# Kernel optimization log

Hardware: AMD Instinct MI355X
Metric: run time of the kernel (lower is better)

The kernel has to match this reference:

```python
import math
import jax, jax.numpy as jnp
import numpy as np

H = 16  # head_count

def setup_inputs() -> dict:
    key = jax.random.key(0)
    ks = jax.random.split(key, 7)
    B, S, D = 2, 2048, 1024
    query = jax.random.normal(ks[0], (B, S, D), dtype=jnp.float32)
    # mask: True = masked position (matches masked_fill_ semantics)
    mask = jax.random.randint(ks[1], (B, S, S), 0, 2) > 0
    scale = 1.0 / math.sqrt(D)  # xavier-ish init scale
    Wq = jax.random.normal(ks[2], (D, D), dtype=jnp.float32) * scale
    Wk = jax.random.normal(ks[3], (D, D), dtype=jnp.float32) * scale
    Wv = jax.random.normal(ks[4], (D, D), dtype=jnp.float32) * scale
    Wo = jax.random.normal(ks[5], (D, D), dtype=jnp.float32) * scale
    bo = jnp.zeros((D,), dtype=jnp.float32)
    return {"query": query, "mask": mask, "Wq": Wq, "Wk": Wk, "Wv": Wv, "Wo": Wo, "bo": bo}


def reference(query, mask, Wq, Wk, Wv, Wo, bo):
    B, S, D = query.shape
    dh = D // H

    def split_heads(x):  # [B,S,D] -> [B,H,S,dh]
        return x.reshape(B, S, H, dh).transpose(0, 2, 1, 3)

    # torch nn.Linear computes x @ W.T (bias-free for q/k/v)
    q = split_heads(query @ Wq.T) * (1.0 / math.sqrt(dh))
    k = split_heads(query @ Wk.T)
    v = split_heads(query @ Wv.T)

    scores = jnp.einsum('bhqd,bhkd->bhqk', q, k)           # [B,H,S,S]
    scores = jnp.where(mask[:, None, :, :], jnp.float32(-1e18), scores)
    weights = jax.nn.softmax(scores, axis=-1)               # dropout=0 -> identity
    ctx = jnp.einsum('bhqk,bhkd->bhqd', weights, v)         # [B,H,S,dh]
    ctx = ctx.transpose(0, 2, 1, 3).reshape(B, S, D)        # combine heads
    return ctx @ Wo.T + bo
```

## Files before the change

### kernel.cpp

```cpp
#include <hip/hip_runtime.h>

#define S_LEN 2048
#define D_MODEL 1024
#define NH 16
#define DH 64

typedef __bf16 bf16x8 __attribute__((ext_vector_type(8)));
typedef __bf16 bf16x4 __attribute__((ext_vector_type(4)));
typedef float f32x4 __attribute__((ext_vector_type(4)));
typedef unsigned short us8 __attribute__((ext_vector_type(8)));

__device__ __forceinline__ unsigned short f2bf(float f) {
  unsigned int x = __float_as_uint(f);
  x += 0x7fffu + ((x >> 16) & 1u);
  return (unsigned short)(x >> 16);
}

__device__ __forceinline__ bf16x4 cvt4(f32x4 v) {
  return __builtin_convertvector(v, bf16x4);
}

__device__ __forceinline__ float exp2raw(float x) {
#if __has_builtin(__builtin_amdgcn_exp2f)
  return __builtin_amdgcn_exp2f(x);
#else
  return exp2f(x);
#endif
}

__device__ __forceinline__ f32x4 mfma16(bf16x8 a, bf16x8 b, f32x4 c) {
  return __builtin_amdgcn_mfma_f32_16x16x32_bf16(a, b, c, 0, 0, 0);
}

__device__ __forceinline__ void gl2lds(const unsigned short* g, unsigned short* l) {
  __builtin_amdgcn_global_load_lds(
      (__attribute__((address_space(1))) void*)g,
      (__attribute__((address_space(3))) void*)l, 16, 0, 0);
}

__global__ __launch_bounds__(256) void prep_kernel(
    const float* __restrict__ q, const float* __restrict__ wq,
    const float* __restrict__ wk, const float* __restrict__ wv,
    const float* __restrict__ wo, const int* __restrict__ mask,
    unsigned short* __restrict__ qbf, unsigned short* __restrict__ wbf,
    unsigned long long* __restrict__ bits) {
  const int bx = blockIdx.x;
  if (bx < 32768) {
    int i = bx * 256 + threadIdx.x;
    unsigned long long bal = __ballot(mask[i] != 0);
    if ((threadIdx.x & 63) == 0) bits[i >> 6] = bal;
  } else {
    const long t = (long)(bx - 32768) * 256 + threadIdx.x;
    const float* src;
    unsigned short* dst;
    long e;
    if (t < 524288) { src = q; dst = qbf; e = t * 8; }
    else {
      long u = t - 524288;
      int wi = (int)(u >> 17);
      e = (u & 131071) * 8;
      src = wi == 0 ? wq : wi == 1 ? wk : wi == 2 ? wv : wo;
      dst = wbf + (long)wi * 1048576;
    }
    float4 a = *(const float4*)(src + e);
    float4 b = *(const float4*)(src + e + 4);
    ushort4 p0 = {f2bf(a.x), f2bf(a.y), f2bf(a.z), f2bf(a.w)};
    ushort4 p1 = {f2bf(b.x), f2bf(b.y), f2bf(b.z), f2bf(b.w)};
    *(ushort4*)(dst + e) = p0;
    *(ushort4*)(dst + e + 4) = p1;
  }
}

__global__ __launch_bounds__(256) void gemm_qkv(
    const unsigned short* __restrict__ A, const unsigned short* __restrict__ W3,
    unsigned short* __restrict__ qb, unsigned short* __restrict__ kb,
    unsigned short* __restrict__ vt, float qscale) {
  __shared__ __align__(16) char smemq[34816];
  unsigned short* As = (unsigned short*)smemq;
  unsigned short* Bs = (unsigned short*)(smemq + 16384);
  unsigned short* E = (unsigned short*)smemq;
  const int tid = threadIdx.x, lane = tid & 63, wid = tid >> 6;
  const int wm = wid >> 1, wn = wid & 1;
  const int quad = lane >> 4, c = lane & 15, cx = c & 7;
  const int nG = blockIdx.x * 128;
  const int wi = nG >> 10, nn0 = nG & 1023;
  const int m0 = blockIdx.y * 128;
  const unsigned short* Bsrc = W3 + (size_t)wi * 1048576;
  const int srow = lane >> 3;
  const int schk = ((lane & 7) ^ srow) * 8;
  const unsigned short* ag = A + (size_t)(m0 + wid * 32 + srow) * 1024 + schk;
  const unsigned short* bg = Bsrc + (size_t)(nn0 + wid * 32 + srow) * 1024 + schk;
  f32x4 acc[4][4] = {};
  for (int kk = 0; kk < 1024; kk += 64) {
#pragma unroll
    for (int i = 0; i < 4; ++i) {
      gl2lds(ag + (size_t)(i * 8) * 1024 + kk, &As[(wid * 32 + i * 8) * 64]);
      gl2lds(bg + (size_t)(i * 8) * 1024 + kk, &Bs[(wid * 32 + i * 8) * 64]);
    }
    __syncthreads();
#pragma unroll
    for (int kc = 0; kc < 2; ++kc) {
      bf16x8 a[4], b[4];
#pragma unroll
      for (int mt = 0; mt < 4; ++mt)
        a[mt] = *(const bf16x8*)(
            &As[(wm * 64 + mt * 16 + c) * 64 + ((kc * 4 + quad) ^ cx) * 8]);
#pragma unroll
      for (int nt = 0; nt < 4; ++nt)
        b[nt] = *(const bf16x8*)(
            &Bs[(wn * 64 + nt * 16 + c) * 64 + ((kc * 4 + quad) ^ cx) * 8]);
#pragma unroll
      for (int mt = 0; mt < 4; ++mt)
#pragma unroll
        for (int nt = 0; nt < 4; ++nt)
          acc[mt][nt] = mfma16(a[mt], b[nt], acc[mt][nt]);
    }
    __syncthreads();
  }

  const float scl = (wi == 0) ? qscale : 1.0f;
  if (wi < 2) {
#pragma unroll
    for (int mt = 0; mt < 4; ++mt)
#pragma unroll
      for (int nt = 0; nt < 4; ++nt) {
        const int sl = wm * 64 + mt * 16 + quad * 4;
        const int nl = wn * 64 + nt * 16 + c;
#pragma unroll
        for (int r = 0; r < 4; ++r)
          E[(sl + r) * 136 + nl] = f2bf(acc[mt][nt][r] * scl);
      }
  } else {
#pragma unroll
    for (int mt = 0; mt < 4; ++mt)
#pragma unroll
      for (int nt = 0; nt < 4; ++nt) {
        const int sl = wm * 64 + mt * 16 + quad * 4;
        const int nl = wn * 64 + nt * 16 + c;
        *(bf16x4*)(&E[nl * 136 + sl]) = cvt4(acc[mt][nt]);
      }
  }
  __syncthreads();
  {
    const int rl = tid >> 1, hf = tid & 1;
    const unsigned short* src = &E[rl * 136 + hf * 64];
    if (wi < 2) {
      const int mb = m0 + rl;
      const int bb = mb >> 11, ss = mb & 2047;
      const int hh = (nn0 + hf * 64) >> 6;
      unsigned short* dst = (wi == 0 ? qb : kb) +
                            (size_t)((bb * NH + hh) * S_LEN + ss) * DH;
#pragma unroll
      for (int j = 0; j < 8; ++j)
        *(us8*)(dst + j * 8) = *(const us8*)(src + j * 8);
    } else {
      const int n = nn0 + rl;
      const int hh = n >> 6, d = n & 63;
      const int bb = m0 >> 11, ss0 = (m0 & 2047) + hf * 64;
      unsigned short* dst =
          vt + (size_t)((bb * NH + hh) * DH + d) * S_LEN + ss0;
#pragma unroll
      for (int j = 0; j < 8; ++j)
        *(us8*)(dst + j * 8) = *(const us8*)(src + j * 8);
    }
  }
}

__global__ __launch_bounds__(256) void gemm_out(
    const unsigned short* __restrict__ A, const unsigned short* __restrict__ W,
    float* __restrict__ out, const float* __restrict__ bias) {
  __shared__ unsigned short As[128 * 128];
  __shared__ unsigned short Bs[64 * 128];
  const int tid = threadIdx.x, lane = tid & 63, wid = tid >> 6;
  const int wm = wid >> 1, wn = wid & 1;
  const int quad = lane >> 4, c = lane & 15, cx = c & 7;
  const int n0 = blockIdx.x * 64, m0 = blockIdx.y * 128;
  const int srow4 = lane >> 4, sch = lane & 15;
  const int co0 = (sch ^ srow4) * 8;
  const int co1 = (sch ^ (4 + srow4)) * 8;
  const unsigned short* agr = A + (size_t)(m0 + wid * 32 + srow4) * 1024;
  const unsigned short* bgr = W + (size_t)(n0 + wid * 16 + srow4) * 1024;
  f32x4 acc[4][2] = {};
  for (int kk = 0; kk < 1024; kk += 128) {
#pragma unroll
    for (int i = 0; i < 8; ++i)
      gl2lds(agr + (size_t)(i * 4) * 1024 + kk + ((i & 1) ? co1 : co0),
             &As[(wid * 32 + i * 4) * 128]);
#pragma unroll
    for (int i = 0; i < 4; ++i)
      gl2lds(bgr + (size_t)(i * 4) * 1024 + kk + ((i & 1) ? co1 : co0),
             &Bs[(wid * 16 + i * 4) * 128]);
    __syncthreads();
#pragma unroll
    for (int kc = 0; kc < 4; ++kc) {
      bf16x8 a[4], b[2];
#pragma unroll
      for (int mt = 0; mt < 4; ++mt)
        a[mt] = *(const bf16x8*)(
            &As[(wm * 64 + mt * 16 + c) * 128 + ((kc * 4 + quad) ^ cx) * 8]);
#pragma unroll
      for (int nt = 0; nt < 2; ++nt)
        b[nt] = *(const bf16x8*)(
            &Bs[(wn * 32 + nt * 16 + c) * 128 + ((kc * 4 + quad) ^ cx) * 8]);
#pragma unroll
      for (int mt = 0; mt < 4; ++mt)
#pragma unroll
        for (int nt = 0; nt < 2; ++nt)
          acc[mt][nt] = mfma16(a[mt], b[nt], acc[mt][nt]);
    }
    __syncthreads();
  }
#pragma unroll
  for (int mt = 0; mt < 4; ++mt) {
#pragma unroll
    for (int nt = 0; nt < 2; ++nt) {
      const int mb = m0 + wm * 64 + mt * 16 + quad * 4;
      const int n = n0 + wn * 32 + nt * 16 + c;
      const float bv = bias[n];
#pragma unroll
      for (int r = 0; r < 4; ++r)
        out[(size_t)(mb + r) * D_MODEL + n] = acc[mt][nt][r] + bv;
    }
  }
}

__global__ __launch_bounds__(256, 2) void attn_kernel(
    const unsigned short* __restrict__ qb, const unsigned short* __restrict__ kb,
    const unsigned short* __restrict__ vt,
    const unsigned long long* __restrict__ mbits,
    unsigned short* __restrict__ ctx) {
  const int h = blockIdx.x, qt = blockIdx.y, b = blockIdx.z;
  const int bh = b * NH + h;
  const int tid = threadIdx.x, lane = tid & 63, wid = tid >> 6;
  const int quad = lane >> 4, c = lane & 15, cx = c & 7;
  const int qw = wid & 1, kh = wid >> 1;
  const int q0 = qt * 128;
  __shared__ __align__(16) char smem[65536];
  unsigned short* KVb = (unsigned short*)smem;

  const int qbase = q0 + qw * 64;
  const unsigned short* qp = qb + (size_t)(bh * S_LEN + qbase + c) * DH;
  bf16x8 bq[4][2];
#pragma unroll
  for (int sub = 0; sub < 4; ++sub) {
    bq[sub][0] = *(const bf16x8*)(qp + sub * 16 * DH + quad * 8);
    bq[sub][1] = *(const bf16x8*)(qp + sub * 16 * DH + 32 + quad * 8);
  }

  const bf16x8 onesv = {(__bf16)1.f, (__bf16)1.f, (__bf16)1.f, (__bf16)1.f,
                        (__bf16)1.f, (__bf16)1.f, (__bf16)1.f, (__bf16)1.f};

  f32x4 o[4][4] = {};
  float lacc[4] = {0.f, 0.f, 0.f, 0.f};
  const unsigned long long* mq0 =
      mbits + (size_t)(b * S_LEN + qbase + c) * 32 + kh * 16;

  const int srow = lane >> 3, schk = ((lane & 7) ^ srow) * 8;

  const unsigned short* gKb =
      kb + (size_t)(bh * S_LEN + (wid & 1) * 1024) * DH + schk;
  const unsigned short* gV =
      vt + (size_t)(bh * DH + srow) * S_LEN + (wid - 2) * 1024 + schk;

  for (int kt = 0; kt < 1024; kt += 128) {
    if (wid < 2) {
#pragma unroll
      for (int hf = 0; hf < 2; ++hf)
#pragma unroll
        for (int i = 0; i < 8; ++i) {
          const int t = i * 8 + srow;
          const int st = (t & 0x23) | ((t >> 2) & 0x04) | ((t << 1) & 0x18);
          gl2lds(gKb + (size_t)(kt + hf * 64 + st) * DH,
                 &KVb[hf * 16384 + wid * 4096 + i * 512]);
        }
    } else {
#pragma unroll
      for (int hf = 0; hf < 2; ++hf)
#pragma unroll
        for (int i = 0; i < 8; ++i)
          gl2lds(gV + (size_t)(i * 8) * S_LEN + kt + hf * 64,
                 &KVb[hf * 16384 + wid * 4096 + i * 512]);
    }
    __syncthreads();

#pragma unroll
    for (int hf = 0; hf < 2; ++hf) {
      const unsigned short* Ksh = KVb + hf * 16384 + kh * 4096;
      const unsigned short* Vsh = KVb + hf * 16384 + (2 + kh) * 4096;
      const int mi = (kt >> 6) + hf;

      bf16x8 kf[8];
#pragma unroll
      for (int g = 0; g < 4; ++g) {
        const int rho = g * 16 + c;
        kf[2 * g] = *(const bf16x8*)(&Ksh[rho * 64 + (quad ^ cx) * 8]);
        kf[2 * g + 1] =
            *(const bf16x8*)(&Ksh[rho * 64 + ((4 + quad) ^ cx) * 8]);
      }

      bf16x8 bps[4][2];
#pragma unroll
      for (int sub = 0; sub < 4; ++sub) {
        f32x4 s[4];
        __builtin_amdgcn_s_setprio(1);
#pragma unroll
        for (int g = 0; g < 4; ++g) {
          f32x4 z = {};
          z = mfma16(kf[2 * g], bq[sub][0], z);
          z = mfma16(kf[2 * g + 1], bq[sub][1], z);
          s[g] = z;
        }
        __builtin_amdgcn_s_setprio(0);
        const unsigned long long w64 = mq0[sub * 512 + mi];
        const unsigned int wlo = (unsigned int)w64;
        const unsigned int whi = (unsigned int)(w64 >> 32);
        f32x4 p[4];
#pragma unroll
        for (int g = 0; g < 4; ++g) {
          const unsigned int bits =
              ((g & 2) ? whi : wlo) >> (quad * 8 + (g & 1) * 4);
#pragma unroll
          for (int r = 0; r < 4; ++r) {
            const float e = exp2raw(s[g][r]);
            p[g][r] = ((bits >> r) & 1u) ? 0.f : e;
          }
        }
        union { bf16x8 v; bf16x4 h[2]; } u0, u1;
        u0.h[0] = cvt4(p[0]); u0.h[1] = cvt4(p[1]);
        u1.h[0] = cvt4(p[2]); u1.h[1] = cvt4(p[3]);
        bps[sub][0] = u0.v;
        bps[sub][1] = u1.v;
        f32x4 zs = {};
        zs = mfma16(onesv, bps[sub][0], zs);
        zs = mfma16(onesv, bps[sub][1], zs);
        lacc[sub] += zs[0];
      }

      __builtin_amdgcn_s_setprio(1);
#pragma unroll
      for (int ks = 0; ks < 2; ++ks) {
#pragma unroll
        for (int nt = 0; nt < 4; ++nt) {
          bf16x8 av = *(const bf16x8*)(
              &Vsh[(nt * 16 + c) * 64 + ((ks * 4 + quad) ^ cx) * 8]);
#pragma unroll
          for (int sub = 0; sub < 4; ++sub)
            o[sub][nt] = mfma16(av, bps[sub][ks], o[sub][nt]);
        }
      }
      __builtin_amdgcn_s_setprio(0);
    }
    __syncthreads();
  }

  float* mrg = (float*)smem;
  float* ml = mrg + 8 * 1088;
  if (kh == 1) {
#pragma unroll
    for (int sub = 0; sub < 4; ++sub) {
      float* mo = mrg + (qw * 4 + sub) * 1088;
#pragma unroll
      for (int nt = 0; nt < 4; ++nt)
        *(f32x4*)(mo + c * 68 + nt * 16 + quad * 4) = o[sub][nt];
      if (quad == 0) ml[(qw * 4 + sub) * 16 + c] = lacc[sub];
    }
  }
  __syncthreads();
  if (kh == 0) {
#pragma unroll
    for (int sub = 0; sub < 4; ++sub) {
      const int pp = qw * 4 + sub;
      const float inv = 1.0f / (lacc[sub] + ml[pp * 16 + c]);
      const int q = qbase + sub * 16 + c;
      const float* mo = mrg + pp * 1088;
#pragma unroll
      for (int nt = 0; nt < 4; ++nt) {
        f32x4 ob = *(const f32x4*)(mo + c * 68 + nt * 16 + quad * 4);
        f32x4 rr = (o[sub][nt] + ob) * inv;
        *(bf16x4*)(ctx + (size_t)(b * S_LEN + q) * D_MODEL + h * DH + nt * 16 +
                   quad * 4) = cvt4(rr);
      }
    }
  }
}

extern "C" void kernel_launch(void* const* d_in, const int* in_sizes, int n_in,
                              void* d_out, int out_size, void* d_ws, size_t ws_size,
                              hipStream_t stream) {
  const float* query = (const float*)d_in[0];
  const int* mask = (const int*)d_in[1];
  const float* Wq = (const float*)d_in[2];
  const float* Wk = (const float*)d_in[3];
  const float* Wv = (const float*)d_in[4];
  const float* Wo = (const float*)d_in[5];
  const float* bo = (const float*)d_in[6];
  float* out = (float*)d_out;

  char* ws = (char*)d_ws;
  const size_t MB = 1024 * 1024;
  unsigned short* qbf = (unsigned short*)(ws);
  unsigned short* wbf = (unsigned short*)(ws + 8 * MB);
  unsigned short* qb = (unsigned short*)(ws + 16 * MB);
  unsigned short* kb = (unsigned short*)(ws + 24 * MB);
  unsigned short* vt = (unsigned short*)(ws + 32 * MB);
  unsigned long long* mb = (unsigned long long*)(ws + 40 * MB);
  unsigned short* ctx = qbf;

  prep_kernel<<<32768 + 4096, 256, 0, stream>>>(query, Wq, Wk, Wv, Wo, mask,
                                                qbf, wbf, mb);

  gemm_qkv<<<dim3(3072 / 128, 4096 / 128), 256, 0, stream>>>(
      qbf, wbf, qb, kb, vt, 0.18033688f);

  attn_kernel<<<dim3(NH, S_LEN / 128, 2), 256, 0, stream>>>(qb, kb, vt, mb,
                                                            ctx);

  gemm_out<<<dim3(1024 / 64, 4096 / 128), 256, 0, stream>>>(
      ctx, wbf + 3 * 1048576, out, bo);
}
```

Before: 219.5 us.

## Fold mask bit-packing into QKV GEMM main loop to overlap with compute

Moves the mask-to-bitmask ballot packing out of the prep kernel and distributes it across the QKV GEMM blocks, each handling up to 43 chunks of 256 mask ints spread over its k-loop iterations. The 32 MB int mask read is meant to overlap with the GEMM's MFMA work instead of running as a separate bandwidth-bound phase. The risk is extra register pressure and memory traffic inside the GEMM loop that may slow the matmul itself.

```diff
diff --git a/kernel.cpp b/kernel.cpp
--- a/kernel.cpp
+++ b/kernel.cpp
@@ -41,40 +41,33 @@
 __global__ __launch_bounds__(256) void prep_kernel(
     const float* __restrict__ q, const float* __restrict__ wq,
     const float* __restrict__ wk, const float* __restrict__ wv,
-    const float* __restrict__ wo, const int* __restrict__ mask,
-    unsigned short* __restrict__ qbf, unsigned short* __restrict__ wbf,
-    unsigned long long* __restrict__ bits) {
-  const int bx = blockIdx.x;
-  if (bx < 32768) {
-    int i = bx * 256 + threadIdx.x;
-    unsigned long long bal = __ballot(mask[i] != 0);
-    if ((threadIdx.x & 63) == 0) bits[i >> 6] = bal;
-  } else {
-    const long t = (long)(bx - 32768) * 256 + threadIdx.x;
-    const float* src;
-    unsigned short* dst;
-    long e;
-    if (t < 524288) { src = q; dst = qbf; e = t * 8; }
-    else {
-      long u = t - 524288;
-      int wi = (int)(u >> 17);
-      e = (u & 131071) * 8;
-      src = wi == 0 ? wq : wi == 1 ? wk : wi == 2 ? wv : wo;
-      dst = wbf + (long)wi * 1048576;
-    }
-    float4 a = *(const float4*)(src + e);
-    float4 b = *(const float4*)(src + e + 4);
-    ushort4 p0 = {f2bf(a.x), f2bf(a.y), f2bf(a.z), f2bf(a.w)};
-    ushort4 p1 = {f2bf(b.x), f2bf(b.y), f2bf(b.z), f2bf(b.w)};
-    *(ushort4*)(dst + e) = p0;
-    *(ushort4*)(dst + e + 4) = p1;
-  }
+    const float* __restrict__ wo, unsigned short* __restrict__ qbf,
+    unsigned short* __restrict__ wbf) {
+  const long t = (long)blockIdx.x * 256 + threadIdx.x;
+  const float* src;
+  unsigned short* dst;
+  long e;
+  if (t < 524288) { src = q; dst = qbf; e = t * 8; }
+  else {
+    long u = t - 524288;
+    int wi = (int)(u >> 17);
+    e = (u & 131071) * 8;
+    src = wi == 0 ? wq : wi == 1 ? wk : wi == 2 ? wv : wo;
+    dst = wbf + (long)wi * 1048576;
+  }
+  float4 a = *(const float4*)(src + e);
+  float4 b = *(const float4*)(src + e + 4);
+  ushort4 p0 = {f2bf(a.x), f2bf(a.y), f2bf(a.z), f2bf(a.w)};
+  ushort4 p1 = {f2bf(b.x), f2bf(b.y), f2bf(b.z), f2bf(b.w)};
+  *(ushort4*)(dst + e) = p0;
+  *(ushort4*)(dst + e + 4) = p1;
 }
 
 __global__ __launch_bounds__(256) void gemm_qkv(
     const unsigned short* __restrict__ A, const unsigned short* __restrict__ W3,
     unsigned short* __restrict__ qb, unsigned short* __restrict__ kb,
-    unsigned short* __restrict__ vt, float qscale) {
+    unsigned short* __restrict__ vt, const int* __restrict__ mask,
+    unsigned long long* __restrict__ bits, float qscale) {
   __shared__ __align__(16) char smemq[34816];
   unsigned short* As = (unsigned short*)smemq;
   unsigned short* Bs = (unsigned short*)(smemq + 16384);
@@ -85,6 +78,7 @@
   const int nG = blockIdx.x * 128;
   const int wi = nG >> 10, nn0 = nG & 1023;
   const int m0 = blockIdx.y * 128;
+  const int bid = blockIdx.y * 24 + blockIdx.x;
   const unsigned short* Bsrc = W3 + (size_t)wi * 1048576;
   const int srow = lane >> 3;
   const int schk = ((lane & 7) ^ srow) * 8;
@@ -92,12 +86,29 @@
   const unsigned short* bg = Bsrc + (size_t)(nn0 + wid * 32 + srow) * 1024 + schk;
   f32x4 acc[4][4] = {};
   for (int kk = 0; kk < 1024; kk += 64) {
+    const int it = kk >> 6;
+    int mv[3], uu[3];
+    bool mok[3];
+#pragma unroll
+    for (int k = 0; k < 3; ++k) {
+      const int loc = it * 3 + k;
+      uu[k] = bid * 43 + loc;
+      mok[k] = (loc < 43) && (uu[k] < 32768);
+      mv[k] = 0;
+      if (mok[k]) mv[k] = mask[(size_t)uu[k] * 256 + tid];
+    }
 #pragma unroll
     for (int i = 0; i < 4; ++i) {
       gl2lds(ag + (size_t)(i * 8) * 1024 + kk, &As[(wid * 32 + i * 8) * 64]);
       gl2lds(bg + (size_t)(i * 8) * 1024 + kk, &Bs[(wid * 32 + i * 8) * 64]);
     }
     __syncthreads();
+#pragma unroll
+    for (int k = 0; k < 3; ++k)
+      if (mok[k]) {
+        unsigned long long bal = __ballot(mv[k] != 0);
+        if ((tid & 63) == 0) bits[(size_t)uu[k] * 4 + (tid >> 6)] = bal;
+      }
 #pragma unroll
     for (int kc = 0; kc < 2; ++kc) {
       bf16x8 a[4], b[4];
@@ -406,11 +417,10 @@
   unsigned long long* mb = (unsigned long long*)(ws + 40 * MB);
   unsigned short* ctx = qbf;
 
-  prep_kernel<<<32768 + 4096, 256, 0, stream>>>(query, Wq, Wk, Wv, Wo, mask,
-                                                qbf, wbf, mb);
+  prep_kernel<<<4096, 256, 0, stream>>>(query, Wq, Wk, Wv, Wo, qbf, wbf);
 
   gemm_qkv<<<dim3(3072 / 128, 4096 / 128), 256, 0, stream>>>(
-      qbf, wbf, qb, kb, vt, 0.18033688f);
+      qbf, wbf, qb, kb, vt, mask, mb, 0.18033688f);
 
   attn_kernel<<<dim3(NH, S_LEN / 128, 2), 256, 0, stream>>>(qb, kb, vt, mb,
                                                             ctx);
```

New measurement: 221.1 us. About the same (+0.8%).
